# Performance work log

Measured on AMD Instinct MI355X. Metric: run time of the kernel, lower is better.

The kernel has to match this reference:

```python
import jax, jax.numpy as jnp
import numpy as np

N = 100000
E = 3200000
F_IN = 128
HID = 64
NUM_GRAPHS = 512
NUM_CLASSES = 2


def setup_inputs() -> dict:
    key = jax.random.key(0)
    ks = jax.random.split(key, 8)
    x = jax.random.normal(ks[0], (N, F_IN), dtype=jnp.float32)
    edge_index = jax.random.randint(ks[1], (2, E), 0, N, dtype=jnp.int64)
    batch = jnp.sort(jax.random.randint(ks[2], (N,), 0, NUM_GRAPHS, dtype=jnp.int64))
    # Glorot-style init for GCN weights, PyTorch default-style for fc
    W1 = jax.random.normal(ks[3], (F_IN, HID), dtype=jnp.float32) * (1.0 / np.sqrt(F_IN))
    b1 = jnp.zeros((HID,), dtype=jnp.float32)
    W2 = jax.random.normal(ks[4], (HID, HID), dtype=jnp.float32) * (1.0 / np.sqrt(HID))
    b2 = jnp.zeros((HID,), dtype=jnp.float32)
    Wfc = jax.random.normal(ks[5], (HID, NUM_CLASSES), dtype=jnp.float32) * (1.0 / np.sqrt(HID))
    bfc = jax.random.normal(ks[6], (NUM_CLASSES,), dtype=jnp.float32) * 0.01
    return {"x": x, "edge_index": edge_index, "batch": batch,
            "W1": W1, "b1": b1, "W2": W2, "b2": b2, "Wfc": Wfc, "bfc": bfc}


def _gcn_conv(x, row, col, deg_inv_sqrt, W, b):
    """PyG GCNConv: out[col] += d^{-1/2}[row] d^{-1/2}[col] * (x W)[row], self-loops included in row/col."""
    h = x @ W  # [N, out_dim]
    norm = deg_inv_sqrt[row] * deg_inv_sqrt[col]  # [E+N]
    msgs = h[row] * norm[:, None]  # gather + scale
    out = jax.ops.segment_sum(msgs, col, num_segments=N)  # scatter-add
    return out + b


def reference(x, edge_index, batch, W1, b1, W2, b2, Wfc, bfc):
    # add self-loops once (shared normalization for both layers)
    loop = jnp.arange(N, dtype=edge_index.dtype)
    row = jnp.concatenate([edge_index[0], loop])  # sources
    col = jnp.concatenate([edge_index[1], loop])  # targets
    deg = jax.ops.segment_sum(jnp.ones_like(col, dtype=x.dtype), col, num_segments=N)
    deg_inv_sqrt = jnp.where(deg > 0, jax.lax.rsqrt(deg), 0.0)

    h = jax.nn.relu(_gcn_conv(x, row, col, deg_inv_sqrt, W1, b1))
    h = jax.nn.relu(_gcn_conv(h, row, col, deg_inv_sqrt, W2, b2))

    # global_mean_pool over batch ids
    sums = jax.ops.segment_sum(h, batch, num_segments=NUM_GRAPHS)  # [G, HID]
    counts = jax.ops.segment_sum(jnp.ones((N,), dtype=h.dtype), batch, num_segments=NUM_GRAPHS)
    pooled = sums / jnp.maximum(counts, 1.0)[:, None]

    # dropout p=0.5 is identity in eval mode
    return pooled @ Wfc + bfc  # [G, NUM_CLASSES]
```

## Files before the change

kernel.cpp:

```cpp
#include <hip/hip_runtime.h>

#define N_NODES   100000
#define N_EDGES   3200000
#define F_INP     128
#define HID       64
#define N_GRAPHS  512
#define N_CLASSES 2
#define NB        782
#define SCAT_BLOCKS 256
#define CHUNK     (N_EDGES / SCAT_BLOCKS)

__device__ __forceinline__ unsigned short f2bf(float f) {
    unsigned int u = __float_as_uint(f);
    return (unsigned short)((u + 0x7FFFu + ((u >> 16) & 1u)) >> 16);
}
__device__ __forceinline__ float bf_lo(unsigned int u) { return __uint_as_float(u << 16); }
__device__ __forceinline__ float bf_hi(unsigned int u) { return __uint_as_float(u & 0xFFFF0000u); }

__global__ __launch_bounds__(256) void hist_kernel(const int* __restrict__ ei,
                                                   int* __restrict__ bcnt) {
    __shared__ int hist[NB];
    for (int i = threadIdx.x; i < NB; i += 256) hist[i] = 0;
    __syncthreads();
    const int e0 = blockIdx.x * CHUNK, e1 = e0 + CHUNK;
    for (int e = e0 + threadIdx.x; e < e1; e += 256)
        atomicAdd(&hist[ei[N_EDGES + e] >> 7], 1);
    __syncthreads();
    for (int i = threadIdx.x; i < NB; i += 256)
        if (hist[i]) atomicAdd(&bcnt[i], hist[i]);
}

__global__ __launch_bounds__(1024) void scan_kernel(const int* __restrict__ bcnt,
                                                    int* __restrict__ boff,
                                                    int* __restrict__ gcur) {
    __shared__ int s[1024];
    const int tid = threadIdx.x;
    const int v = (tid < NB) ? bcnt[tid] : 0;
    s[tid] = v;
    __syncthreads();
    for (int d = 1; d < 1024; d <<= 1) {
        int t = (tid >= d) ? s[tid - d] : 0;
        __syncthreads();
        s[tid] += t;
        __syncthreads();
    }
    if (tid <= NB) {
        int ex = s[tid] - v;
        boff[tid] = ex;
        if (tid < NB) gcur[tid] = ex;
    }
}

__global__ __launch_bounds__(256) void scatter_kernel(const int* __restrict__ ei,
                                                      int* __restrict__ gcur,
                                                      int* __restrict__ pairs) {
    __shared__ int hist[NB];
    __shared__ int lbase[NB];
    __shared__ int lcur[NB];
    for (int i = threadIdx.x; i < NB; i += 256) { hist[i] = 0; lcur[i] = 0; }
    __syncthreads();
    const int e0 = blockIdx.x * CHUNK, e1 = e0 + CHUNK;
    for (int e = e0 + threadIdx.x; e < e1; e += 256)
        atomicAdd(&hist[ei[N_EDGES + e] >> 7], 1);
    __syncthreads();
    for (int i = threadIdx.x; i < NB; i += 256)
        lbase[i] = hist[i] ? atomicAdd(&gcur[i], hist[i]) : 0;
    __syncthreads();
    for (int e = e0 + threadIdx.x; e < e1; e += 256) {
        int c = ei[N_EDGES + e];
        int r = ei[e];
        int b = c >> 7;
        int off = atomicAdd(&lcur[b], 1);
        pairs[lbase[b] + off] = r | ((c & 127) << 17);
    }
}

__global__ __launch_bounds__(256) void csr_kernel(const int* __restrict__ pairs,
                                                  const int* __restrict__ boff,
                                                  int* __restrict__ adj,
                                                  int* __restrict__ offs,
                                                  float* __restrict__ dis) {
    __shared__ int cnt[128];
    __shared__ int sc[128];
    __shared__ int base[128];
    __shared__ int cur[128];
    const int tid = threadIdx.x;
    const int b = blockIdx.x;
    const int beg = boff[b], end = boff[b + 1];
    if (tid < 128) { cnt[tid] = 0; cur[tid] = 0; }
    __syncthreads();
    for (int e = beg + tid; e < end; e += 256)
        atomicAdd(&cnt[pairs[e] >> 17], 1);
    __syncthreads();
    if (tid < 128) sc[tid] = cnt[tid];
    __syncthreads();
    for (int d = 1; d < 128; d <<= 1) {
        int t = (tid >= d && tid < 128) ? sc[tid - d] : 0;
        __syncthreads();
        if (tid < 128) sc[tid] += t;
        __syncthreads();
    }
    if (tid < 128) base[tid] = beg + sc[tid] - cnt[tid];
    __syncthreads();
    for (int e = beg + tid; e < end; e += 256) {
        int v = pairs[e];
        int lc = v >> 17;
        int o = atomicAdd(&cur[lc], 1);
        adj[base[lc] + o] = v & 131071;
    }
    const int n = (b << 7) + tid;
    if (tid < 128 && n < N_NODES) {
        offs[n] = base[tid];
        dis[n] = rsqrtf((float)cnt[tid] + 1.0f);
    }
    if (b == 0 && tid == 0) offs[N_NODES] = N_EDGES;
}

__global__ void counts_kernel(const int* __restrict__ batch, int* __restrict__ counts) {
    const int g = blockIdx.x * blockDim.x + threadIdx.x;
    if (g >= N_GRAPHS) return;
    int lo = 0, hi = N_NODES;
    while (lo < hi) { int m = (lo + hi) >> 1; if (batch[m] < g) lo = m + 1; else hi = m; }
    const int l0 = lo;
    lo = 0; hi = N_NODES;
    while (lo < hi) { int m = (lo + hi) >> 1; if (batch[m] < g + 1) lo = m + 1; else hi = m; }
    counts[g] = lo - l0;
}

__global__ __launch_bounds__(256) void mm1_kernel(const float* __restrict__ x,
                                                  const float* __restrict__ W1,
                                                  const float* __restrict__ dis,
                                                  unsigned short* __restrict__ p) {
    __shared__ float ws[F_INP * HID];
    for (int i = threadIdx.x; i < F_INP * HID / 4; i += 256)
        ((float4*)ws)[i] = ((const float4*)W1)[i];
    __syncthreads();
    const int tx = threadIdx.x & 15;
    const int ty = threadIdx.x >> 4;
    const int row0 = blockIdx.x * 64 + ty * 4;
    int r[4];
#pragma unroll
    for (int i = 0; i < 4; ++i) r[i] = min(row0 + i, N_NODES - 1);
    float acc[4][4] = {};
#pragma unroll 2
    for (int k = 0; k < F_INP; k += 4) {
        float4 a[4];
#pragma unroll
        for (int i = 0; i < 4; ++i)
            a[i] = *(const float4*)(x + (size_t)r[i] * F_INP + k);
        float4 w0 = *(const float4*)(ws + (k + 0) * HID + tx * 4);
        float4 w1 = *(const float4*)(ws + (k + 1) * HID + tx * 4);
        float4 w2 = *(const float4*)(ws + (k + 2) * HID + tx * 4);
        float4 w3 = *(const float4*)(ws + (k + 3) * HID + tx * 4);
#pragma unroll
        for (int i = 0; i < 4; ++i) {
            acc[i][0] += a[i].x * w0.x + a[i].y * w1.x + a[i].z * w2.x + a[i].w * w3.x;
            acc[i][1] += a[i].x * w0.y + a[i].y * w1.y + a[i].z * w2.y + a[i].w * w3.y;
            acc[i][2] += a[i].x * w0.z + a[i].y * w1.z + a[i].z * w2.z + a[i].w * w3.z;
            acc[i][3] += a[i].x * w0.w + a[i].y * w1.w + a[i].z * w2.w + a[i].w * w3.w;
        }
    }
#pragma unroll
    for (int i = 0; i < 4; ++i) {
        int rr = row0 + i;
        if (rr < N_NODES) {
            float d = dis[rr];
            ushort4 o;
            o.x = f2bf(d * acc[i][0]);
            o.y = f2bf(d * acc[i][1]);
            o.z = f2bf(d * acc[i][2]);
            o.w = f2bf(d * acc[i][3]);
            *(ushort4*)(p + (size_t)rr * HID + tx * 4) = o;
        }
    }
}

__global__ __launch_bounds__(256) void mm2_kernel(const float* __restrict__ h,
                                                  const float* __restrict__ W2,
                                                  const float* __restrict__ dis,
                                                  unsigned short* __restrict__ p) {
    __shared__ float ws[HID * HID];
    for (int i = threadIdx.x; i < HID * HID / 4; i += 256)
        ((float4*)ws)[i] = ((const float4*)W2)[i];
    __syncthreads();
    const int tx = threadIdx.x & 15;
    const int ty = threadIdx.x >> 4;
    const int row0 = blockIdx.x * 64 + ty * 4;
    int r[4];
#pragma unroll
    for (int i = 0; i < 4; ++i) r[i] = min(row0 + i, N_NODES - 1);
    float acc[4][4] = {};
#pragma unroll 2
    for (int k = 0; k < HID; k += 4) {
        float4 a[4];
#pragma unroll
        for (int i = 0; i < 4; ++i)
            a[i] = *(const float4*)(h + (size_t)r[i] * HID + k);
        float4 w0 = *(const float4*)(ws + (k + 0) * HID + tx * 4);
        float4 w1 = *(const float4*)(ws + (k + 1) * HID + tx * 4);
        float4 w2 = *(const float4*)(ws + (k + 2) * HID + tx * 4);
        float4 w3 = *(const float4*)(ws + (k + 3) * HID + tx * 4);
#pragma unroll
        for (int i = 0; i < 4; ++i) {
            acc[i][0] += a[i].x * w0.x + a[i].y * w1.x + a[i].z * w2.x + a[i].w * w3.x;
            acc[i][1] += a[i].x * w0.y + a[i].y * w1.y + a[i].z * w2.y + a[i].w * w3.y;
            acc[i][2] += a[i].x * w0.z + a[i].y * w1.z + a[i].z * w2.z + a[i].w * w3.z;
            acc[i][3] += a[i].x * w0.w + a[i].y * w1.w + a[i].z * w2.w + a[i].w * w3.w;
        }
    }
#pragma unroll
    for (int i = 0; i < 4; ++i) {
        int rr = row0 + i;
        if (rr < N_NODES) {
            float d = dis[rr];
            ushort4 o;
            o.x = f2bf(d * acc[i][0]);
            o.y = f2bf(d * acc[i][1]);
            o.z = f2bf(d * acc[i][2]);
            o.w = f2bf(d * acc[i][3]);
            *(ushort4*)(p + (size_t)rr * HID + tx * 4) = o;
        }
    }
}

__device__ __forceinline__ float gather_node(const unsigned short* __restrict__ p,
                                             const int* __restrict__ adj,
                                             int c, int beg, int end, int q, int g) {
    float acc[8];
    {
        uint4 s = *(const uint4*)(p + (size_t)c * HID + g * 8);
        float sm = (q == 0) ? 1.f : 0.f;
        acc[0] = sm * bf_lo(s.x); acc[1] = sm * bf_hi(s.x);
        acc[2] = sm * bf_lo(s.y); acc[3] = sm * bf_hi(s.y);
        acc[4] = sm * bf_lo(s.z); acc[5] = sm * bf_hi(s.z);
        acc[6] = sm * bf_lo(s.w); acc[7] = sm * bf_hi(s.w);
    }
    int e = beg;
    for (; e + 16 <= end; e += 16) {
        int r0 = adj[e + q];
        int r1 = adj[e + 8 + q];
        uint4 v0 = *(const uint4*)(p + (size_t)r0 * HID + g * 8);
        uint4 v1 = *(const uint4*)(p + (size_t)r1 * HID + g * 8);
        acc[0] += bf_lo(v0.x) + bf_lo(v1.x); acc[1] += bf_hi(v0.x) + bf_hi(v1.x);
        acc[2] += bf_lo(v0.y) + bf_lo(v1.y); acc[3] += bf_hi(v0.y) + bf_hi(v1.y);
        acc[4] += bf_lo(v0.z) + bf_lo(v1.z); acc[5] += bf_hi(v0.z) + bf_hi(v1.z);
        acc[6] += bf_lo(v0.w) + bf_lo(v1.w); acc[7] += bf_hi(v0.w) + bf_hi(v1.w);
    }
    for (; e < end; e += 8) {
        int idx = e + q;
        int r = adj[min(idx, end - 1)];
        float m = (idx < end) ? 1.f : 0.f;
        uint4 v = *(const uint4*)(p + (size_t)r * HID + g * 8);
        acc[0] = fmaf(m, bf_lo(v.x), acc[0]); acc[1] = fmaf(m, bf_hi(v.x), acc[1]);
        acc[2] = fmaf(m, bf_lo(v.y), acc[2]); acc[3] = fmaf(m, bf_hi(v.y), acc[3]);
        acc[4] = fmaf(m, bf_lo(v.z), acc[4]); acc[5] = fmaf(m, bf_hi(v.z), acc[5]);
        acc[6] = fmaf(m, bf_lo(v.w), acc[6]); acc[7] = fmaf(m, bf_hi(v.w), acc[7]);
    }
#pragma unroll
    for (int j = 0; j < 8; ++j) {
        acc[j] += __shfl_xor(acc[j], 8, 64);
        acc[j] += __shfl_xor(acc[j], 16, 64);
        acc[j] += __shfl_xor(acc[j], 32, 64);
    }
    return (q & 4) ? ((q & 2) ? ((q & 1) ? acc[7] : acc[6]) : ((q & 1) ? acc[5] : acc[4]))
                   : ((q & 2) ? ((q & 1) ? acc[3] : acc[2]) : ((q & 1) ? acc[1] : acc[0]));
}

__global__ __launch_bounds__(256) void gather1_kernel(const unsigned short* __restrict__ p,
                                                      const int* __restrict__ adj,
                                                      const int* __restrict__ offs,
                                                      const float* __restrict__ dis,
                                                      const float* __restrict__ b1,
                                                      float* __restrict__ h) {
    const int lane = threadIdx.x & 63;
    const int q = lane >> 3, g = lane & 7;
    const int gwave = (blockIdx.x * blockDim.x + threadIdx.x) >> 6;
    const int nwaves = (gridDim.x * blockDim.x) >> 6;
    const float bj = b1[g * 8 + q];
    for (int c = gwave; c < N_NODES; c += nwaves) {
        const int beg = offs[c], end = offs[c + 1];
        float val = gather_node(p, adj, c, beg, end, q, g);
        h[(size_t)c * HID + g * 8 + q] = fmaxf(dis[c] * val + bj, 0.f);
    }
}

__global__ __launch_bounds__(256) void gather2_kernel(const unsigned short* __restrict__ p,
                                                      const int* __restrict__ adj,
                                                      const int* __restrict__ offs,
                                                      const float* __restrict__ dis,
                                                      const float* __restrict__ b2,
                                                      const int* __restrict__ batch,
                                                      float* __restrict__ sums) {
    const int lane = threadIdx.x & 63;
    const int q = lane >> 3, g = lane & 7;
    const int gwave = (blockIdx.x * blockDim.x + threadIdx.x) >> 6;
    const int nwaves = (gridDim.x * blockDim.x) >> 6;
    const float bj = b2[g * 8 + q];
    for (int c = gwave; c < N_NODES; c += nwaves) {
        const int beg = offs[c], end = offs[c + 1];
        float val = gather_node(p, adj, c, beg, end, q, g);
        float v = fmaxf(dis[c] * val + bj, 0.f);
        atomicAdd(&sums[(size_t)batch[c] * HID + g * 8 + q], v);
    }
}

__global__ void fc_kernel(const float* __restrict__ sums, const int* __restrict__ counts,
                          const float* __restrict__ Wfc, const float* __restrict__ bfc,
                          float* __restrict__ out) {
    const int g = blockIdx.x;
    const int j = threadIdx.x;
    float cnt = fmaxf((float)counts[g], 1.0f);
    float pj = sums[(size_t)g * HID + j] / cnt;
    float a0 = pj * Wfc[j * N_CLASSES + 0];
    float a1 = pj * Wfc[j * N_CLASSES + 1];
    for (int off = 32; off > 0; off >>= 1) {
        a0 += __shfl_down(a0, off, 64);
        a1 += __shfl_down(a1, off, 64);
    }
    if (j == 0) {
        out[g * N_CLASSES + 0] = a0 + bfc[0];
        out[g * N_CLASSES + 1] = a1 + bfc[1];
    }
}

extern "C" void kernel_launch(void* const* d_in, const int* in_sizes, int n_in,
                              void* d_out, int out_size, void* d_ws, size_t ws_size,
                              hipStream_t stream) {
    const float* x     = (const float*)d_in[0];
    const int*   ei    = (const int*)d_in[1];
    const int*   batch = (const int*)d_in[2];
    const float* W1    = (const float*)d_in[3];
    const float* b1    = (const float*)d_in[4];
    const float* W2    = (const float*)d_in[5];
    const float* b2    = (const float*)d_in[6];
    const float* Wfc   = (const float*)d_in[7];
    const float* bfc   = (const float*)d_in[8];
    float* out = (float*)d_out;

    char* ws = (char*)d_ws;
    size_t off = 0;
    auto alloc = [&](size_t bytes) -> void* {
        void* pp = ws + off;
        off += (bytes + 255) & ~(size_t)255;
        return pp;
    };
    int*   bcnt   = (int*)alloc((size_t)NB * 4);
    int*   boff   = (int*)alloc((size_t)(NB + 1) * 4);
    int*   gcur   = (int*)alloc((size_t)NB * 4);
    float* dis    = (float*)alloc((size_t)N_NODES * 4);
    int*   pairs  = (int*)alloc((size_t)N_EDGES * 4);
    int*   adj    = (int*)alloc((size_t)N_EDGES * 4);
    int*   offs   = (int*)alloc((size_t)(N_NODES + 1) * 4);
    unsigned short* p = (unsigned short*)alloc((size_t)N_NODES * HID * 2);
    float* h      = (float*)alloc((size_t)N_NODES * HID * 4);
    float* sums   = (float*)alloc((size_t)N_GRAPHS * HID * 4);
    int*   counts = (int*)alloc((size_t)N_GRAPHS * 4);

    hipMemsetAsync(bcnt, 0, (size_t)NB * 4, stream);
    hipMemsetAsync(sums, 0, (size_t)N_GRAPHS * HID * 4, stream);

    hist_kernel<<<SCAT_BLOCKS, 256, 0, stream>>>(ei, bcnt);
    scan_kernel<<<1, 1024, 0, stream>>>(bcnt, boff, gcur);
    scatter_kernel<<<SCAT_BLOCKS, 256, 0, stream>>>(ei, gcur, pairs);
    csr_kernel<<<NB, 256, 0, stream>>>(pairs, boff, adj, offs, dis);
    counts_kernel<<<2, 256, 0, stream>>>(batch, counts);
    mm1_kernel<<<(N_NODES + 63) / 64, 256, 0, stream>>>(x, W1, dis, p);
    gather1_kernel<<<2048, 256, 0, stream>>>(p, adj, offs, dis, b1, h);
    mm2_kernel<<<(N_NODES + 63) / 64, 256, 0, stream>>>(h, W2, dis, p);
    gather2_kernel<<<2048, 256, 0, stream>>>(p, adj, offs, dis, b2, batch, sums);
    fc_kernel<<<N_GRAPHS, 64, 0, stream>>>(sums, counts, Wfc, bfc, out);
}
```

Baseline: 386.7 us.

## Precompute per-block bucket bases, store hidden layer in bf16, unroll gather

```diff
diff --git a/kernel.cpp b/kernel.cpp
--- a/kernel.cpp
+++ b/kernel.cpp
@@ -18,7 +18,8 @@
 __device__ __forceinline__ float bf_hi(unsigned int u) { return __uint_as_float(u & 0xFFFF0000u); }
 
 __global__ __launch_bounds__(256) void hist_kernel(const int* __restrict__ ei,
-                                                   int* __restrict__ bcnt) {
+                                                   int* __restrict__ bcnt,
+                                                   int* __restrict__ bh) {
     __shared__ int hist[NB];
     for (int i = threadIdx.x; i < NB; i += 256) hist[i] = 0;
     __syncthreads();
@@ -26,13 +27,15 @@
     for (int e = e0 + threadIdx.x; e < e1; e += 256)
         atomicAdd(&hist[ei[N_EDGES + e] >> 7], 1);
     __syncthreads();
-    for (int i = threadIdx.x; i < NB; i += 256)
-        if (hist[i]) atomicAdd(&bcnt[i], hist[i]);
+    for (int i = threadIdx.x; i < NB; i += 256) {
+        int v = hist[i];
+        bh[(size_t)blockIdx.x * NB + i] = v;
+        if (v) atomicAdd(&bcnt[i], v);
+    }
 }
 
 __global__ __launch_bounds__(1024) void scan_kernel(const int* __restrict__ bcnt,
-                                                    int* __restrict__ boff,
-                                                    int* __restrict__ gcur) {
+                                                    int* __restrict__ boff) {
     __shared__ int s[1024];
     const int tid = threadIdx.x;
     const int v = (tid < NB) ? bcnt[tid] : 0;
@@ -44,28 +47,37 @@
         s[tid] += t;
         __syncthreads();
     }
-    if (tid <= NB) {
-        int ex = s[tid] - v;
-        boff[tid] = ex;
-        if (tid < NB) gcur[tid] = ex;
-    }
+    if (tid <= NB) boff[tid] = s[tid] - v;
+}
+
+__global__ __launch_bounds__(256) void bbase_kernel(int* __restrict__ bh,
+                                                    const int* __restrict__ boff) {
+    __shared__ int s[256];
+    const int b = blockIdx.x;
+    const int tid = threadIdx.x;
+    const int v = bh[(size_t)tid * NB + b];
+    s[tid] = v;
+    __syncthreads();
+    for (int d = 1; d < 256; d <<= 1) {
+        int t = (tid >= d) ? s[tid - d] : 0;
+        __syncthreads();
+        s[tid] += t;
+        __syncthreads();
+    }
+    bh[(size_t)tid * NB + b] = boff[b] + s[tid] - v;
 }
 
 __global__ __launch_bounds__(256) void scatter_kernel(const int* __restrict__ ei,
-                                                      int* __restrict__ gcur,
+                                                      const int* __restrict__ bh,
                                                       int* __restrict__ pairs) {
-    __shared__ int hist[NB];
     __shared__ int lbase[NB];
     __shared__ int lcur[NB];
-    for (int i = threadIdx.x; i < NB; i += 256) { hist[i] = 0; lcur[i] = 0; }
+    for (int i = threadIdx.x; i < NB; i += 256) {
+        lbase[i] = bh[(size_t)blockIdx.x * NB + i];
+        lcur[i] = 0;
+    }
     __syncthreads();
     const int e0 = blockIdx.x * CHUNK, e1 = e0 + CHUNK;
-    for (int e = e0 + threadIdx.x; e < e1; e += 256)
-        atomicAdd(&hist[ei[N_EDGES + e] >> 7], 1);
-    __syncthreads();
-    for (int i = threadIdx.x; i < NB; i += 256)
-        lbase[i] = hist[i] ? atomicAdd(&gcur[i], hist[i]) : 0;
-    __syncthreads();
     for (int e = e0 + threadIdx.x; e < e1; e += 256) {
         int c = ei[N_EDGES + e];
         int r = ei[e];
@@ -175,7 +187,7 @@
     }
 }
 
-__global__ __launch_bounds__(256) void mm2_kernel(const float* __restrict__ h,
+__global__ __launch_bounds__(256) void mm2_kernel(const unsigned short* __restrict__ hb,
                                                   const float* __restrict__ W2,
                                                   const float* __restrict__ dis,
                                                   unsigned short* __restrict__ p) {
@@ -191,21 +203,29 @@
     for (int i = 0; i < 4; ++i) r[i] = min(row0 + i, N_NODES - 1);
     float acc[4][4] = {};
 #pragma unroll 2
-    for (int k = 0; k < HID; k += 4) {
-        float4 a[4];
+    for (int k = 0; k < HID; k += 8) {
+        uint4 a[4];
 #pragma unroll
         for (int i = 0; i < 4; ++i)
-            a[i] = *(const float4*)(h + (size_t)r[i] * HID + k);
-        float4 w0 = *(const float4*)(ws + (k + 0) * HID + tx * 4);
-        float4 w1 = *(const float4*)(ws + (k + 1) * HID + tx * 4);
-        float4 w2 = *(const float4*)(ws + (k + 2) * HID + tx * 4);
-        float4 w3 = *(const float4*)(ws + (k + 3) * HID + tx * 4);
+            a[i] = *(const uint4*)(hb + (size_t)r[i] * HID + k);
+        float4 w[8];
+#pragma unroll
+        for (int m = 0; m < 8; ++m)
+            w[m] = *(const float4*)(ws + (k + m) * HID + tx * 4);
 #pragma unroll
         for (int i = 0; i < 4; ++i) {
-            acc[i][0] += a[i].x * w0.x + a[i].y * w1.x + a[i].z * w2.x + a[i].w * w3.x;
-            acc[i][1] += a[i].x * w0.y + a[i].y * w1.y + a[i].z * w2.y + a[i].w * w3.y;
-            acc[i][2] += a[i].x * w0.z + a[i].y * w1.z + a[i].z * w2.z + a[i].w * w3.z;
-            acc[i][3] += a[i].x * w0.w + a[i].y * w1.w + a[i].z * w2.w + a[i].w * w3.w;
+            float h0 = bf_lo(a[i].x), h1 = bf_hi(a[i].x);
+            float h2 = bf_lo(a[i].y), h3 = bf_hi(a[i].y);
+            float h4 = bf_lo(a[i].z), h5 = bf_hi(a[i].z);
+            float h6 = bf_lo(a[i].w), h7 = bf_hi(a[i].w);
+            acc[i][0] += h0 * w[0].x + h1 * w[1].x + h2 * w[2].x + h3 * w[3].x
+                       + h4 * w[4].x + h5 * w[5].x + h6 * w[6].x + h7 * w[7].x;
+            acc[i][1] += h0 * w[0].y + h1 * w[1].y + h2 * w[2].y + h3 * w[3].y
+                       + h4 * w[4].y + h5 * w[5].y + h6 * w[6].y + h7 * w[7].y;
+            acc[i][2] += h0 * w[0].z + h1 * w[1].z + h2 * w[2].z + h3 * w[3].z
+                       + h4 * w[4].z + h5 * w[5].z + h6 * w[6].z + h7 * w[7].z;
+            acc[i][3] += h0 * w[0].w + h1 * w[1].w + h2 * w[2].w + h3 * w[3].w
+                       + h4 * w[4].w + h5 * w[5].w + h6 * w[6].w + h7 * w[7].w;
         }
     }
 #pragma unroll
@@ -236,6 +256,24 @@
         acc[6] = sm * bf_lo(s.w); acc[7] = sm * bf_hi(s.w);
     }
     int e = beg;
+    for (; e + 32 <= end; e += 32) {
+        int r0 = adj[e + q];
+        int r1 = adj[e + 8 + q];
+        int r2 = adj[e + 16 + q];
+        int r3 = adj[e + 24 + q];
+        uint4 v0 = *(const uint4*)(p + (size_t)r0 * HID + g * 8);
+        uint4 v1 = *(const uint4*)(p + (size_t)r1 * HID + g * 8);
+        uint4 v2 = *(const uint4*)(p + (size_t)r2 * HID + g * 8);
+        uint4 v3 = *(const uint4*)(p + (size_t)r3 * HID + g * 8);
+        acc[0] += (bf_lo(v0.x) + bf_lo(v1.x)) + (bf_lo(v2.x) + bf_lo(v3.x));
+        acc[1] += (bf_hi(v0.x) + bf_hi(v1.x)) + (bf_hi(v2.x) + bf_hi(v3.x));
+        acc[2] += (bf_lo(v0.y) + bf_lo(v1.y)) + (bf_lo(v2.y) + bf_lo(v3.y));
+        acc[3] += (bf_hi(v0.y) + bf_hi(v1.y)) + (bf_hi(v2.y) + bf_hi(v3.y));
+        acc[4] += (bf_lo(v0.z) + bf_lo(v1.z)) + (bf_lo(v2.z) + bf_lo(v3.z));
+        acc[5] += (bf_hi(v0.z) + bf_hi(v1.z)) + (bf_hi(v2.z) + bf_hi(v3.z));
+        acc[6] += (bf_lo(v0.w) + bf_lo(v1.w)) + (bf_lo(v2.w) + bf_lo(v3.w));
+        acc[7] += (bf_hi(v0.w) + bf_hi(v1.w)) + (bf_hi(v2.w) + bf_hi(v3.w));
+    }
     for (; e + 16 <= end; e += 16) {
         int r0 = adj[e + q];
         int r1 = adj[e + 8 + q];
@@ -271,7 +309,7 @@
                                                       const int* __restrict__ offs,
                                                       const float* __restrict__ dis,
                                                       const float* __restrict__ b1,
-                                                      float* __restrict__ h) {
+                                                      unsigned short* __restrict__ hb) {
     const int lane = threadIdx.x & 63;
     const int q = lane >> 3, g = lane & 7;
     const int gwave = (blockIdx.x * blockDim.x + threadIdx.x) >> 6;
@@ -280,7 +318,7 @@
     for (int c = gwave; c < N_NODES; c += nwaves) {
         const int beg = offs[c], end = offs[c + 1];
         float val = gather_node(p, adj, c, beg, end, q, g);
-        h[(size_t)c * HID + g * 8 + q] = fmaxf(dis[c] * val + bj, 0.f);
+        hb[(size_t)c * HID + g * 8 + q] = f2bf(fmaxf(dis[c] * val + bj, 0.f));
     }
 }
 
@@ -346,27 +384,28 @@
     };
     int*   bcnt   = (int*)alloc((size_t)NB * 4);
     int*   boff   = (int*)alloc((size_t)(NB + 1) * 4);
-    int*   gcur   = (int*)alloc((size_t)NB * 4);
+    int*   bh     = (int*)alloc((size_t)SCAT_BLOCKS * NB * 4);
     float* dis    = (float*)alloc((size_t)N_NODES * 4);
     int*   pairs  = (int*)alloc((size_t)N_EDGES * 4);
     int*   adj    = (int*)alloc((size_t)N_EDGES * 4);
     int*   offs   = (int*)alloc((size_t)(N_NODES + 1) * 4);
-    unsigned short* p = (unsigned short*)alloc((size_t)N_NODES * HID * 2);
-    float* h      = (float*)alloc((size_t)N_NODES * HID * 4);
+    unsigned short* p  = (unsigned short*)alloc((size_t)N_NODES * HID * 2);
+    unsigned short* hb = (unsigned short*)alloc((size_t)N_NODES * HID * 2);
     float* sums   = (float*)alloc((size_t)N_GRAPHS * HID * 4);
     int*   counts = (int*)alloc((size_t)N_GRAPHS * 4);
 
     hipMemsetAsync(bcnt, 0, (size_t)NB * 4, stream);
     hipMemsetAsync(sums, 0, (size_t)N_GRAPHS * HID * 4, stream);
 
-    hist_kernel<<<SCAT_BLOCKS, 256, 0, stream>>>(ei, bcnt);
-    scan_kernel<<<1, 1024, 0, stream>>>(bcnt, boff, gcur);
-    scatter_kernel<<<SCAT_BLOCKS, 256, 0, stream>>>(ei, gcur, pairs);
+    hist_kernel<<<SCAT_BLOCKS, 256, 0, stream>>>(ei, bcnt, bh);
+    scan_kernel<<<1, 1024, 0, stream>>>(bcnt, boff);
+    bbase_kernel<<<NB, 256, 0, stream>>>(bh, boff);
+    scatter_kernel<<<SCAT_BLOCKS, 256, 0, stream>>>(ei, bh, pairs);
     csr_kernel<<<NB, 256, 0, stream>>>(pairs, boff, adj, offs, dis);
     counts_kernel<<<2, 256, 0, stream>>>(batch, counts);
     mm1_kernel<<<(N_NODES + 63) / 64, 256, 0, stream>>>(x, W1, dis, p);
-    gather1_kernel<<<2048, 256, 0, stream>>>(p, adj, offs, dis, b1, h);
-    mm2_kernel<<<(N_NODES + 63) / 64, 256, 0, stream>>>(h, W2, dis, p);
+    gather1_kernel<<<2048, 256, 0, stream>>>(p, adj, offs, dis, b1, hb);
+    mm2_kernel<<<(N_NODES + 63) / 64, 256, 0, stream>>>(hb, W2, dis, p);
     gather2_kernel<<<2048, 256, 0, stream>>>(p, adj, offs, dis, b2, batch, sums);
     fc_kernel<<<N_GRAPHS, 64, 0, stream>>>(sums, counts, Wfc, bfc, out);
 }
```

New measurement: 388.0 us. About the same (+0.3%).
